# Kernel tuning notes

Measured on AMD Instinct MI355X. Metric: run time of the kernel, lower is better.

The kernel has to match this reference:

```python
import jax, jax.numpy as jnp
import numpy as np

H = 32          # phasor harmonics
DELTA0 = 7.0    # base phasor frequency
HID = 128       # hidden_dim
NEXP = 4        # num_experts
EDIM = 64       # expert_dim
NCLS = 3        # num_classes
IN_DIM = 28 * 28
ENH_DIM = HID + 2 * H  # 192


def setup_inputs() -> dict:
    key = jax.random.key(0)
    ks = jax.random.split(key, 12)
    B = 65536
    s = lambda d: 1.0 / np.sqrt(d)
    return {
        "x": jax.random.normal(ks[0], (B, 28, 28), dtype=jnp.float32),
        "W_in": jax.random.normal(ks[1], (IN_DIM, HID), dtype=jnp.float32) * s(IN_DIM),
        "b_in": jnp.zeros((HID,), dtype=jnp.float32),
        "W_gate": jax.random.normal(ks[2], (ENH_DIM, NEXP), dtype=jnp.float32) * s(ENH_DIM),
        "b_gate": jnp.zeros((NEXP,), dtype=jnp.float32),
        "W_exp": jax.random.normal(ks[3], (NEXP, ENH_DIM, EDIM), dtype=jnp.float32) * s(ENH_DIM),
        "b_exp": jnp.zeros((NEXP, EDIM), dtype=jnp.float32),
        "W_ctx": jax.random.normal(ks[4], (EDIM, HID), dtype=jnp.float32) * s(EDIM),
        "b_ctx": jnp.zeros((HID,), dtype=jnp.float32),
        "W_out": jax.random.normal(ks[5], (HID, NCLS), dtype=jnp.float32) * s(HID),
        "b_out": jnp.zeros((NCLS,), dtype=jnp.float32),
    }


def _phasor_bank(t):
    # t: [B] scalar drive per sample -> [B, 2H] cos/sin harmonic features
    freqs = DELTA0 * jnp.arange(1, H + 1, dtype=t.dtype)  # [H]
    phase = t[:, None] * freqs[None, :]                   # [B, H]
    return jnp.concatenate([jnp.cos(phase), jnp.sin(phase)], axis=-1)


def reference(x, W_in, b_in, W_gate, b_gate, W_exp, b_exp, W_ctx, b_ctx, W_out, b_out):
    B = x.shape[0]
    x_flat = x.reshape((B, -1))                                  # [B, 784]
    projected = x_flat @ W_in + b_in                             # [B, HID]
    t = jnp.mean(projected, axis=-1)                             # [B]
    temporal = _phasor_bank(t)                                   # [B, 2H]
    enhanced = jnp.concatenate([projected, temporal], axis=-1)   # [B, ENH_DIM]
    # Expert retrieval core: softmax gate over NEXP experts
    gate = jax.nn.softmax(enhanced @ W_gate + b_gate, axis=-1)   # [B, NEXP]
    expert_out = jax.nn.relu(
        jnp.einsum('bd,edh->beh', enhanced, W_exp) + b_exp[None] # [B, NEXP, EDIM]
    )
    combined = jnp.einsum('be,beh->bh', gate, expert_out)        # [B, EDIM]
    context = jnp.tanh(combined @ W_ctx + b_ctx)                 # [B, HID]
    logits = context @ W_out + b_out                             # [B, NCLS]
    return logits
```

## Files before the change

kernel.cpp:

```cpp
#include <hip/hip_runtime.h>

typedef unsigned short u16;
typedef unsigned int u32;
typedef __attribute__((ext_vector_type(8))) short short8;
typedef __attribute__((ext_vector_type(4))) float f32x4;

#define OFF_WM    0
#define OFF_WINF  3584
#define OFF_WEGF  208384
#define OFF_WCTXF 312832
#define OFF_WOUTF 329216

__device__ __forceinline__ u16 f2bf(float x) {
  union { float f; u32 u; } v; v.f = x;
  u32 r = v.u + 0x7FFFu + ((v.u >> 16) & 1u);
  return (u16)(r >> 16);
}

__global__ void prep_kernel(const float* __restrict__ W_in, const float* __restrict__ b_in,
                            const float* __restrict__ W_gate, const float* __restrict__ W_exp,
                            const float* __restrict__ W_ctx, const float* __restrict__ W_out,
                            float* __restrict__ wm, u16* __restrict__ WinF,
                            u16* __restrict__ WegF, u16* __restrict__ WctxF,
                            u16* __restrict__ WoutF) {
  int idx = blockIdx.x * 256 + threadIdx.x;
  if (idx < 801) {
    if (idx == 800) {
      float s = 0.f;
      for (int j = 0; j < 128; ++j) s += b_in[j];
      wm[800] = s * (1.f / 128.f);
    } else if (idx >= 784) {
      wm[idx] = 0.f;
    } else {
      float s = 0.f;
      for (int j = 0; j < 128; ++j) s += W_in[idx * 128 + j];
      wm[idx] = s * (1.f / 128.f);
    }
  } else if (idx < 103201) {
    int f = idx - 801;
    int j = f & 7, lane = (f >> 3) & 63, tile = f >> 9;
    int ct = tile & 7, kt = tile >> 3;
    int k = kt * 32 + ((lane >> 4) << 3) + j;
    int n = ct * 16 + (lane & 15);
    WinF[f] = (k < 784) ? f2bf(W_in[k * 128 + n]) : (u16)0;
  } else if (idx < 155425) {
    int f = idx - 103201;
    int j = f & 7, lane = (f >> 3) & 63, tile = f >> 9;
    int kt = tile / 17, ct = tile - kt * 17;
    int k = kt * 32 + ((lane >> 4) << 3) + j;
    int n = ct * 16 + (lane & 15);
    float v = 0.f;
    if (n < 256) { int e = n >> 6, h = n & 63; v = W_exp[(e * 192 + k) * 64 + h]; }
    else if (n < 260) v = W_gate[k * 4 + (n - 256)];
    WegF[f] = f2bf(v);
  } else if (idx < 163617) {
    int f = idx - 155425;
    int j = f & 7, lane = (f >> 3) & 63, tile = f >> 9;
    int ct = tile & 7, kt = tile >> 3;
    int k = kt * 32 + ((lane >> 4) << 3) + j;
    int n = ct * 16 + (lane & 15);
    WctxF[f] = f2bf(W_ctx[k * 128 + n]);
  } else if (idx < 165665) {
    int f = idx - 163617;
    int j = f & 7, lane = (f >> 3) & 63, kt = f >> 9;
    int k = kt * 32 + ((lane >> 4) << 3) + j;
    int n = lane & 15;
    WoutF[f] = (n < 3) ? f2bf(W_out[k * 3 + n]) : (u16)0;
  }
}

__global__ __launch_bounds__(256, 2)
void fused_kernel(const float* __restrict__ x,
                  const float* __restrict__ b_in, const float* __restrict__ b_gate,
                  const float* __restrict__ b_exp, const float* __restrict__ b_ctx,
                  const float* __restrict__ b_out,
                  const float* __restrict__ wm, const u16* __restrict__ WinF,
                  const u16* __restrict__ WegF, const u16* __restrict__ WctxF,
                  const u16* __restrict__ WoutF,
                  float* __restrict__ out) {
  __shared__ __align__(16) u16 smem[4 * 7680 + 8192];
  const int tid = threadIdx.x;
  const int wv = tid >> 6;
  const int ln = tid & 63;
  const int cb = ln & 15;
  const int qr = ln >> 4;
  u16* enh0 = smem + wv * 7680;
  u16* enh1 = enh0 + 3840;
  u16* cmb0 = enh0;
  u16* cmb1 = enh1;
  u16* ctx0 = enh0 + 1280;
  u16* ctx1 = enh1 + 1280;
  u16* stg  = smem + 4 * 7680;

  const int grow = blockIdx.x * 128 + wv * 32;
  const float* xr0 = x + (size_t)(grow + cb) * 784;
  const float* xr1 = xr0 + (size_t)16 * 784;

  const f32x4 vz = {0.f, 0.f, 0.f, 0.f};

  f32x4 acc0[8], acc1[8];
  #pragma unroll
  for (int i = 0; i < 8; ++i) { acc0[i] = vz; acc1[i] = vz; }
  float tp0 = 0.f, tp1 = 0.f;

  {
    const u16* src = WinF + tid * 8;
    short8 r0 = *(const short8*)(src);
    short8 r1 = *(const short8*)(src + 2048);
    *(short8*)(stg + tid * 8) = r0;
    *(short8*)(stg + 2048 + tid * 8) = r1;
  }
  __syncthreads();

  for (int kt = 0; kt < 25; ++kt) {
    const int buf = (kt & 1) << 12;
    short8 r0 = short8{0,0,0,0,0,0,0,0}, r1 = r0;
    const bool pf = (kt < 24);
    if (pf) {
      const u16* src = WinF + (size_t)(kt + 1) * 4096 + tid * 8;
      r0 = *(const short8*)(src);
      r1 = *(const short8*)(src + 2048);
    }

    const int k0 = kt * 32 + qr * 8;
    union { short8 s; u32 u[4]; } af, bf;
    {
      float4 a0 = make_float4(0.f, 0.f, 0.f, 0.f), a1 = a0;
      float4 b0 = a0, b1 = a0, m0 = a0, m1 = a0;
      if (k0 < 784) {
        a0 = *(const float4*)(xr0 + k0);
        a1 = *(const float4*)(xr0 + k0 + 4);
        b0 = *(const float4*)(xr1 + k0);
        b1 = *(const float4*)(xr1 + k0 + 4);
        m0 = *(const float4*)(wm + k0);
        m1 = *(const float4*)(wm + k0 + 4);
        tp0 += a0.x * m0.x + a0.y * m0.y + a0.z * m0.z + a0.w * m0.w
             + a1.x * m1.x + a1.y * m1.y + a1.z * m1.z + a1.w * m1.w;
        tp1 += b0.x * m0.x + b0.y * m0.y + b0.z * m0.z + b0.w * m0.w
             + b1.x * m1.x + b1.y * m1.y + b1.z * m1.z + b1.w * m1.w;
      }
      af.u[0] = (u32)f2bf(a0.x) | ((u32)f2bf(a0.y) << 16);
      af.u[1] = (u32)f2bf(a0.z) | ((u32)f2bf(a0.w) << 16);
      af.u[2] = (u32)f2bf(a1.x) | ((u32)f2bf(a1.y) << 16);
      af.u[3] = (u32)f2bf(a1.z) | ((u32)f2bf(a1.w) << 16);
      bf.u[0] = (u32)f2bf(b0.x) | ((u32)f2bf(b0.y) << 16);
      bf.u[1] = (u32)f2bf(b0.z) | ((u32)f2bf(b0.w) << 16);
      bf.u[2] = (u32)f2bf(b1.x) | ((u32)f2bf(b1.y) << 16);
      bf.u[3] = (u32)f2bf(b1.z) | ((u32)f2bf(b1.w) << 16);
    }

    short8 Bf[8];
    #pragma unroll
    for (int ct = 0; ct < 8; ++ct)
      Bf[ct] = *(const short8*)(stg + buf + ct * 512 + ln * 8);

    #pragma unroll
    for (int ct = 0; ct < 8; ++ct) {
      acc0[ct] = __builtin_amdgcn_mfma_f32_16x16x32_bf16(af.s, Bf[ct], acc0[ct], 0, 0, 0);
      acc1[ct] = __builtin_amdgcn_mfma_f32_16x16x32_bf16(bf.s, Bf[ct], acc1[ct], 0, 0, 0);
    }

    if (pf) {
      u16* dst = stg + (buf ^ 4096);
      *(short8*)(dst + tid * 8) = r0;
      *(short8*)(dst + 2048 + tid * 8) = r1;
    }
    __syncthreads();
  }

  tp0 += __shfl_xor(tp0, 16);
  tp0 += __shfl_xor(tp0, 32);
  tp1 += __shfl_xor(tp1, 16);
  tp1 += __shfl_xor(tp1, 32);
  const float mb = wm[800];
  const float t0 = tp0 + mb;
  const float t1 = tp1 + mb;

  #pragma unroll
  for (int ct = 0; ct < 8; ++ct) {
    float bi = b_in[ct * 16 + cb];
    u16* d0 = enh0 + (ct >> 1) * 640 + (ct & 1) * 16 + cb;
    u16* d1 = enh1 + (ct >> 1) * 640 + (ct & 1) * 16 + cb;
    #pragma unroll
    for (int i = 0; i < 4; ++i) {
      d0[(qr * 4 + i) * 40] = f2bf(acc0[ct][i] + bi);
      d1[(qr * 4 + i) * 40] = f2bf(acc1[ct][i] + bi);
    }
  }
  #pragma unroll
  for (int g = 0; g < 2; ++g) {
    float t = g ? t1 : t0;
    u16* eW = g ? enh1 : enh0;
    float phi = 7.f * t;
    float ss, cc, sd, cd;
    sincosf(phi * (float)(qr * 8 + 1), &ss, &cc);
    sincosf(phi, &sd, &cd);
    u16* pc = eW + 4 * 640 + cb * 40 + qr * 8;
    u16* ps = eW + 5 * 640 + cb * 40 + qr * 8;
    #pragma unroll
    for (int m = 0; m < 8; ++m) {
      pc[m] = f2bf(cc);
      ps[m] = f2bf(ss);
      float nc = cc * cd - ss * sd;
      ss = ss * cd + cc * sd;
      cc = nc;
    }
  }

  const u16* gbase = WegF + ln * 8;
  f32x4 g0 = vz, g1 = vz;
  #pragma unroll
  for (int kt = 0; kt < 6; ++kt) {
    short8 A0 = *(const short8*)(enh0 + kt * 640 + cb * 40 + qr * 8);
    short8 A1 = *(const short8*)(enh1 + kt * 640 + cb * 40 + qr * 8);
    short8 Bg = *(const short8*)(gbase + (size_t)(kt * 17 + 16) * 512);
    g0 = __builtin_amdgcn_mfma_f32_16x16x32_bf16(A0, Bg, g0, 0, 0, 0);
    g1 = __builtin_amdgcn_mfma_f32_16x16x32_bf16(A1, Bg, g1, 0, 0, 0);
  }

  float ge0[4][4], ge1[4][4];
  {
    float bg = b_gate[cb & 3];
    #pragma unroll
    for (int i = 0; i < 4; ++i) {
      {
        float gi = g0[i] + bg;
        float mx = fmaxf(gi, __shfl_xor(gi, 1));
        mx = fmaxf(mx, __shfl_xor(mx, 2));
        float ev = __expf(gi - mx);
        float sv = ev + __shfl_xor(ev, 1);
        sv += __shfl_xor(sv, 2);
        float g = ev / sv;
        int base = qr * 16;
        ge0[0][i] = __shfl(g, base + 0);
        ge0[1][i] = __shfl(g, base + 1);
        ge0[2][i] = __shfl(g, base + 2);
        ge0[3][i] = __shfl(g, base + 3);
      }
      {
        float gi = g1[i] + bg;
        float mx = fmaxf(gi, __shfl_xor(gi, 1));
        mx = fmaxf(mx, __shfl_xor(mx, 2));
        float ev = __expf(gi - mx);
        float sv = ev + __shfl_xor(ev, 1);
        sv += __shfl_xor(sv, 2);
        float g = ev / sv;
        int base = qr * 16;
        ge1[0][i] = __shfl(g, base + 0);
        ge1[1][i] = __shfl(g, base + 1);
        ge1[2][i] = __shfl(g, base + 2);
        ge1[3][i] = __shfl(g, base + 3);
      }
    }
  }

  f32x4 ae0[16], ae1[16];
  #pragma unroll
  for (int c = 0; c < 16; ++c) { ae0[c] = vz; ae1[c] = vz; }
  for (int kt = 0; kt < 6; ++kt) {
    __syncthreads();
    {
      const u16* src = WegF + (size_t)kt * 17 * 512 + tid * 8;
      short8 s0 = *(const short8*)(src);
      short8 s1 = *(const short8*)(src + 2048);
      short8 s2 = *(const short8*)(src + 4096);
      short8 s3 = *(const short8*)(src + 6144);
      *(short8*)(stg + tid * 8) = s0;
      *(short8*)(stg + 2048 + tid * 8) = s1;
      *(short8*)(stg + 4096 + tid * 8) = s2;
      *(short8*)(stg + 6144 + tid * 8) = s3;
    }
    __syncthreads();
    short8 A0 = *(const short8*)(enh0 + kt * 640 + cb * 40 + qr * 8);
    short8 A1 = *(const short8*)(enh1 + kt * 640 + cb * 40 + qr * 8);
    #pragma unroll
    for (int c = 0; c < 16; ++c) {
      short8 Bf = *(const short8*)(stg + c * 512 + ln * 8);
      ae0[c] = __builtin_amdgcn_mfma_f32_16x16x32_bf16(A0, Bf, ae0[c], 0, 0, 0);
      ae1[c] = __builtin_amdgcn_mfma_f32_16x16x32_bf16(A1, Bf, ae1[c], 0, 0, 0);
    }
  }

  f32x4 cA[4], cB[4];
  #pragma unroll
  for (int i = 0; i < 4; ++i) { cA[i] = vz; cB[i] = vz; }
  #pragma unroll
  for (int e = 0; e < 4; ++e) {
    #pragma unroll
    for (int c2 = 0; c2 < 4; ++c2) {
      float be = b_exp[e * 64 + c2 * 16 + cb];
      #pragma unroll
      for (int i = 0; i < 4; ++i) {
        cA[c2][i] += ge0[e][i] * fmaxf(ae0[e * 4 + c2][i] + be, 0.f);
        cB[c2][i] += ge1[e][i] * fmaxf(ae1[e * 4 + c2][i] + be, 0.f);
      }
    }
  }
  #pragma unroll
  for (int c2 = 0; c2 < 4; ++c2) {
    u16* d0 = cmb0 + (c2 >> 1) * 640 + (c2 & 1) * 16 + cb;
    u16* d1 = cmb1 + (c2 >> 1) * 640 + (c2 & 1) * 16 + cb;
    #pragma unroll
    for (int i = 0; i < 4; ++i) {
      d0[(qr * 4 + i) * 40] = f2bf(cA[c2][i]);
      d1[(qr * 4 + i) * 40] = f2bf(cB[c2][i]);
    }
  }

  __syncthreads();
  {
    const u16* src = WctxF + tid * 8;
    short8 s0 = *(const short8*)(src);
    short8 s1 = *(const short8*)(src + 2048);
    short8 s2 = *(const short8*)(src + 4096);
    short8 s3 = *(const short8*)(src + 6144);
    *(short8*)(stg + tid * 8) = s0;
    *(short8*)(stg + 2048 + tid * 8) = s1;
    *(short8*)(stg + 4096 + tid * 8) = s2;
    *(short8*)(stg + 6144 + tid * 8) = s3;
  }
  __syncthreads();
  f32x4 c30[8], c31[8];
  #pragma unroll
  for (int i = 0; i < 8; ++i) { c30[i] = vz; c31[i] = vz; }
  #pragma unroll
  for (int kt = 0; kt < 2; ++kt) {
    short8 A0 = *(const short8*)(cmb0 + kt * 640 + cb * 40 + qr * 8);
    short8 A1 = *(const short8*)(cmb1 + kt * 640 + cb * 40 + qr * 8);
    #pragma unroll
    for (int ct = 0; ct < 8; ++ct) {
      short8 Bf = *(const short8*)(stg + (kt * 8 + ct) * 512 + ln * 8);
      c30[ct] = __builtin_amdgcn_mfma_f32_16x16x32_bf16(A0, Bf, c30[ct], 0, 0, 0);
      c31[ct] = __builtin_amdgcn_mfma_f32_16x16x32_bf16(A1, Bf, c31[ct], 0, 0, 0);
    }
  }
  #pragma unroll
  for (int ct = 0; ct < 8; ++ct) {
    float bc = b_ctx[ct * 16 + cb];
    u16* d0 = ctx0 + ct * 16 + cb;
    u16* d1 = ctx1 + ct * 16 + cb;
    #pragma unroll
    for (int i = 0; i < 4; ++i) {
      float v0 = c30[ct][i] + bc;
      float e0 = __expf(2.f * v0);
      d0[(qr * 4 + i) * 136] = f2bf(1.f - 2.f / (e0 + 1.f));
      float v1 = c31[ct][i] + bc;
      float e1 = __expf(2.f * v1);
      d1[(qr * 4 + i) * 136] = f2bf(1.f - 2.f / (e1 + 1.f));
    }
  }

  __syncthreads();
  {
    short8 s0 = *(const short8*)(WoutF + tid * 8);
    *(short8*)(stg + tid * 8) = s0;
  }
  __syncthreads();
  f32x4 a40 = vz, a41 = vz;
  #pragma unroll
  for (int kt = 0; kt < 4; ++kt) {
    short8 A0 = *(const short8*)(ctx0 + cb * 136 + kt * 32 + qr * 8);
    short8 A1 = *(const short8*)(ctx1 + cb * 136 + kt * 32 + qr * 8);
    short8 Bf = *(const short8*)(stg + kt * 512 + ln * 8);
    a40 = __builtin_amdgcn_mfma_f32_16x16x32_bf16(A0, Bf, a40, 0, 0, 0);
    a41 = __builtin_amdgcn_mfma_f32_16x16x32_bf16(A1, Bf, a41, 0, 0, 0);
  }
  if (cb < 3) {
    float bo = b_out[cb];
    #pragma unroll
    for (int i = 0; i < 4; ++i) {
      out[(size_t)(grow + qr * 4 + i) * 3 + cb] = a40[i] + bo;
      out[(size_t)(grow + 16 + qr * 4 + i) * 3 + cb] = a41[i] + bo;
    }
  }
}

extern "C" void kernel_launch(void* const* d_in, const int* in_sizes, int n_in,
                              void* d_out, int out_size, void* d_ws, size_t ws_size,
                              hipStream_t stream) {
  const float* x      = (const float*)d_in[0];
  const float* W_in   = (const float*)d_in[1];
  const float* b_in   = (const float*)d_in[2];
  const float* W_gate = (const float*)d_in[3];
  const float* b_gate = (const float*)d_in[4];
  const float* W_exp  = (const float*)d_in[5];
  const float* b_exp  = (const float*)d_in[6];
  const float* W_ctx  = (const float*)d_in[7];
  const float* b_ctx  = (const float*)d_in[8];
  const float* W_out  = (const float*)d_in[9];
  const float* b_out  = (const float*)d_in[10];
  float* out = (float*)d_out;

  char* ws = (char*)d_ws;
  float* wm  = (float*)(ws + OFF_WM);
  u16* WinF  = (u16*)(ws + OFF_WINF);
  u16* WegF  = (u16*)(ws + OFF_WEGF);
  u16* WctxF = (u16*)(ws + OFF_WCTXF);
  u16* WoutF = (u16*)(ws + OFF_WOUTF);

  const int B = in_sizes[0] / 784;
  prep_kernel<<<648, 256, 0, stream>>>(W_in, b_in, W_gate, W_exp, W_ctx, W_out,
                                       wm, WinF, WegF, WctxF, WoutF);
  fused_kernel<<<B / 128, 256, 0, stream>>>(x, b_in, b_gate, b_exp, b_ctx, b_out,
                                            wm, WinF, WegF, WctxF, WoutF, out);
}
```

Baseline: 328.1 us.

## Pre-convert x to bf16 MFMA layout in a separate high-occupancy kernel

Adds a prepx kernel that reads fp32 x once and writes it as bf16 into workspace, laid out in MFMA A-fragment order. The same kernel computes the per-row mean projection t. The fused kernel then loads ready-made bf16 fragments instead of converting fp32 and accumulating t inside its low-occupancy main loop. The cost is an extra write and read of the roughly 100MB bf16 copy plus one more launch. The old fused path is kept as a fallback when the workspace is too small.

```diff
diff --git a/kernel.cpp b/kernel.cpp
--- a/kernel.cpp
+++ b/kernel.cpp
@@ -10,6 +10,8 @@
 #define OFF_WEGF  208384
 #define OFF_WCTXF 312832
 #define OFF_WOUTF 329216
+#define OFF_T     524288
+#define OFF_XF    1048576
 
 __device__ __forceinline__ u16 f2bf(float x) {
   union { float f; u32 u; } v; v.f = x;
@@ -69,15 +71,52 @@
   }
 }
 
+__global__ __launch_bounds__(256, 8)
+void prepx_kernel(const float* __restrict__ x, const float* __restrict__ wm,
+                  u16* __restrict__ xf, float* __restrict__ t, int nrt) {
+  const int rt = blockIdx.x * 4 + (threadIdx.x >> 6);
+  if (rt >= nrt) return;
+  const int ln = threadIdx.x & 63;
+  const int cb = ln & 15;
+  const int qr = ln >> 4;
+  const int row = rt * 16 + cb;
+  const float* xr = x + (size_t)row * 784;
+  u16* dst = xf + ((size_t)rt * 25 * 64 + ln) * 8;
+
+  float part = 0.f;
+  for (int kt = 0; kt < 25; ++kt) {
+    const int k0 = kt * 32 + qr * 8;
+    union { short8 s; u32 u[4]; } af;
+    if (k0 < 784) {
+      float4 a0 = *(const float4*)(xr + k0);
+      float4 a1 = *(const float4*)(xr + k0 + 4);
+      const float4 m0 = *(const float4*)(wm + k0);
+      const float4 m1 = *(const float4*)(wm + k0 + 4);
+      part += a0.x * m0.x + a0.y * m0.y + a0.z * m0.z + a0.w * m0.w
+            + a1.x * m1.x + a1.y * m1.y + a1.z * m1.z + a1.w * m1.w;
+      af.u[0] = (u32)f2bf(a0.x) | ((u32)f2bf(a0.y) << 16);
+      af.u[1] = (u32)f2bf(a0.z) | ((u32)f2bf(a0.w) << 16);
+      af.u[2] = (u32)f2bf(a1.x) | ((u32)f2bf(a1.y) << 16);
+      af.u[3] = (u32)f2bf(a1.z) | ((u32)f2bf(a1.w) << 16);
+    } else {
+      af.u[0] = 0; af.u[1] = 0; af.u[2] = 0; af.u[3] = 0;
+    }
+    *(short8*)(dst + kt * 512) = af.s;
+  }
+  part += __shfl_xor(part, 16);
+  part += __shfl_xor(part, 32);
+  if (ln < 16) t[row] = part;
+}
+
 __global__ __launch_bounds__(256, 2)
-void fused_kernel(const float* __restrict__ x,
-                  const float* __restrict__ b_in, const float* __restrict__ b_gate,
-                  const float* __restrict__ b_exp, const float* __restrict__ b_ctx,
-                  const float* __restrict__ b_out,
-                  const float* __restrict__ wm, const u16* __restrict__ WinF,
-                  const u16* __restrict__ WegF, const u16* __restrict__ WctxF,
-                  const u16* __restrict__ WoutF,
-                  float* __restrict__ out) {
+void fused_kernel_xf(const u16* __restrict__ xf, const float* __restrict__ t,
+                     const float* __restrict__ b_in, const float* __restrict__ b_gate,
+                     const float* __restrict__ b_exp, const float* __restrict__ b_ctx,
+                     const float* __restrict__ b_out,
+                     const float* __restrict__ wm, const u16* __restrict__ WinF,
+                     const u16* __restrict__ WegF, const u16* __restrict__ WctxF,
+                     const u16* __restrict__ WoutF,
+                     float* __restrict__ out) {
   __shared__ __align__(16) u16 smem[4 * 7680 + 8192];
   const int tid = threadIdx.x;
   const int wv = tid >> 6;
@@ -93,15 +132,15 @@
   u16* stg  = smem + 4 * 7680;
 
   const int grow = blockIdx.x * 128 + wv * 32;
-  const float* xr0 = x + (size_t)(grow + cb) * 784;
-  const float* xr1 = xr0 + (size_t)16 * 784;
+  const int rtA = grow >> 4;
+  const u16* xfA = xf + ((size_t)rtA * 25 * 64 + ln) * 8;
+  const u16* xfB = xfA + (size_t)25 * 512;
 
   const f32x4 vz = {0.f, 0.f, 0.f, 0.f};
 
   f32x4 acc0[8], acc1[8];
   #pragma unroll
   for (int i = 0; i < 8; ++i) { acc0[i] = vz; acc1[i] = vz; }
-  float tp0 = 0.f, tp1 = 0.f;
 
   {
     const u16* src = WinF + tid * 8;
@@ -122,32 +161,8 @@
       r1 = *(const short8*)(src + 2048);
     }
 
-    const int k0 = kt * 32 + qr * 8;
-    union { short8 s; u32 u[4]; } af, bf;
-    {
-      float4 a0 = make_float4(0.f, 0.f, 0.f, 0.f), a1 = a0;
-      float4 b0 = a0, b1 = a0, m0 = a0, m1 = a0;
-      if (k0 < 784) {
-        a0 = *(const float4*)(xr0 + k0);
-        a1 = *(const float4*)(xr0 + k0 + 4);
-        b0 = *(const float4*)(xr1 + k0);
-        b1 = *(const float4*)(xr1 + k0 + 4);
-        m0 = *(const float4*)(wm + k0);
-        m1 = *(const float4*)(wm + k0 + 4);
-        tp0 += a0.x * m0.x + a0.y * m0.y + a0.z * m0.z + a0.w * m0.w
-             + a1.x * m1.x + a1.y * m1.y + a1.z * m1.z + a1.w * m1.w;
-        tp1 += b0.x * m0.x + b0.y * m0.y + b0.z * m0.z + b0.w * m0.w
-             + b1.x * m1.x + b1.y * m1.y + b1.z * m1.z + b1.w * m1.w;
-      }
-      af.u[0] = (u32)f2bf(a0.x) | ((u32)f2bf(a0.y) << 16);
-      af.u[1] = (u32)f2bf(a0.z) | ((u32)f2bf(a0.w) << 16);
-      af.u[2] = (u32)f2bf(a1.x) | ((u32)f2bf(a1.y) << 16);
-      af.u[3] = (u32)f2bf(a1.z) | ((u32)f2bf(a1.w) << 16);
-      bf.u[0] = (u32)f2bf(b0.x) | ((u32)f2bf(b0.y) << 16);
-      bf.u[1] = (u32)f2bf(b0.z) | ((u32)f2bf(b0.w) << 16);
-      bf.u[2] = (u32)f2bf(b1.x) | ((u32)f2bf(b1.y) << 16);
-      bf.u[3] = (u32)f2bf(b1.z) | ((u32)f2bf(b1.w) << 16);
-    }
+    short8 A0 = *(const short8*)(xfA + kt * 512);
+    short8 A1 = *(const short8*)(xfB + kt * 512);
 
     short8 Bf[8];
     #pragma unroll
@@ -156,8 +171,8 @@
 
     #pragma unroll
     for (int ct = 0; ct < 8; ++ct) {
-      acc0[ct] = __builtin_amdgcn_mfma_f32_16x16x32_bf16(af.s, Bf[ct], acc0[ct], 0, 0, 0);
-      acc1[ct] = __builtin_amdgcn_mfma_f32_16x16x32_bf16(bf.s, Bf[ct], acc1[ct], 0, 0, 0);
+      acc0[ct] = __builtin_amdgcn_mfma_f32_16x16x32_bf16(A0, Bf[ct], acc0[ct], 0, 0, 0);
+      acc1[ct] = __builtin_amdgcn_mfma_f32_16x16x32_bf16(A1, Bf[ct], acc1[ct], 0, 0, 0);
     }
 
     if (pf) {
@@ -168,13 +183,9 @@
     __syncthreads();
   }
 
-  tp0 += __shfl_xor(tp0, 16);
-  tp0 += __shfl_xor(tp0, 32);
-  tp1 += __shfl_xor(tp1, 16);
-  tp1 += __shfl_xor(tp1, 32);
   const float mb = wm[800];
-  const float t0 = tp0 + mb;
-  const float t1 = tp1 + mb;
+  const float t0 = t[grow + cb] + mb;
+  const float t1 = t[grow + 16 + cb] + mb;
 
   #pragma unroll
   for (int ct = 0; ct < 8; ++ct) {
@@ -189,9 +200,9 @@
   }
   #pragma unroll
   for (int g = 0; g < 2; ++g) {
-    float t = g ? t1 : t0;
+    float t_ = g ? t1 : t0;
     u16* eW = g ? enh1 : enh0;
-    float phi = 7.f * t;
+    float phi = 7.f * t_;
     float ss, cc, sd, cd;
     sincosf(phi * (float)(qr * 8 + 1), &ss, &cc);
     sincosf(phi, &sd, &cd);
@@ -375,6 +386,312 @@
   }
 }
 
+__global__ __launch_bounds__(256, 2)
+void fused_kernel_x(const float* __restrict__ x,
+                    const float* __restrict__ b_in, const float* __restrict__ b_gate,
+                    const float* __restrict__ b_exp, const float* __restrict__ b_ctx,
+                    const float* __restrict__ b_out,
+                    const float* __restrict__ wm, const u16* __restrict__ WinF,
+                    const u16* __restrict__ WegF, const u16* __restrict__ WctxF,
+                    const u16* __restrict__ WoutF,
+                    float* __restrict__ out) {
+  __shared__ __align__(16) u16 smem[4 * 7680 + 8192];
+  const int tid = threadIdx.x;
+  const int wv = tid >> 6;
+  const int ln = tid & 63;
+  const int cb = ln & 15;
+  const int qr = ln >> 4;
+  u16* enh0 = smem + wv * 7680;
+  u16* enh1 = enh0 + 3840;
+  u16* cmb0 = enh0;
+  u16* cmb1 = enh1;
+  u16* ctx0 = enh0 + 1280;
+  u16* ctx1 = enh1 + 1280;
+  u16* stg  = smem + 4 * 7680;
+
+  const int grow = blockIdx.x * 128 + wv * 32;
+  const float* xr0 = x + (size_t)(grow + cb) * 784;
+  const float* xr1 = xr0 + (size_t)16 * 784;
+
+  const f32x4 vz = {0.f, 0.f, 0.f, 0.f};
+
+  f32x4 acc0[8], acc1[8];
+  #pragma unroll
+  for (int i = 0; i < 8; ++i) { acc0[i] = vz; acc1[i] = vz; }
+  float tp0 = 0.f, tp1 = 0.f;
+
+  {
+    const u16* src = WinF + tid * 8;
+    short8 r0 = *(const short8*)(src);
+    short8 r1 = *(const short8*)(src + 2048);
+    *(short8*)(stg + tid * 8) = r0;
+    *(short8*)(stg + 2048 + tid * 8) = r1;
+  }
+  __syncthreads();
+
+  for (int kt = 0; kt < 25; ++kt) {
+    const int buf = (kt & 1) << 12;
+    short8 r0 = short8{0,0,0,0,0,0,0,0}, r1 = r0;
+    const bool pf = (kt < 24);
+    if (pf) {
+      const u16* src = WinF + (size_t)(kt + 1) * 4096 + tid * 8;
+      r0 = *(const short8*)(src);
+      r1 = *(const short8*)(src + 2048);
+    }
+
+    const int k0 = kt * 32 + qr * 8;
+    union { short8 s; u32 u[4]; } af, bf;
+    {
+      float4 a0 = make_float4(0.f, 0.f, 0.f, 0.f), a1 = a0;
+      float4 b0 = a0, b1 = a0, m0 = a0, m1 = a0;
+      if (k0 < 784) {
+        a0 = *(const float4*)(xr0 + k0);
+        a1 = *(const float4*)(xr0 + k0 + 4);
+        b0 = *(const float4*)(xr1 + k0);
+        b1 = *(const float4*)(xr1 + k0 + 4);
+        m0 = *(const float4*)(wm + k0);
+        m1 = *(const float4*)(wm + k0 + 4);
+        tp0 += a0.x * m0.x + a0.y * m0.y + a0.z * m0.z + a0.w * m0.w
+             + a1.x * m1.x + a1.y * m1.y + a1.z * m1.z + a1.w * m1.w;
+        tp1 += b0.x * m0.x + b0.y * m0.y + b0.z * m0.z + b0.w * m0.w
+             + b1.x * m1.x + b1.y * m1.y + b1.z * m1.z + b1.w * m1.w;
+      }
+      af.u[0] = (u32)f2bf(a0.x) | ((u32)f2bf(a0.y) << 16);
+      af.u[1] = (u32)f2bf(a0.z) | ((u32)f2bf(a0.w) << 16);
+      af.u[2] = (u32)f2bf(a1.x) | ((u32)f2bf(a1.y) << 16);
+      af.u[3] = (u32)f2bf(a1.z) | ((u32)f2bf(a1.w) << 16);
+      bf.u[0] = (u32)f2bf(b0.x) | ((u32)f2bf(b0.y) << 16);
+      bf.u[1] = (u32)f2bf(b0.z) | ((u32)f2bf(b0.w) << 16);
+      bf.u[2] = (u32)f2bf(b1.x) | ((u32)f2bf(b1.y) << 16);
+      bf.u[3] = (u32)f2bf(b1.z) | ((u32)f2bf(b1.w) << 16);
+    }
+
+    short8 Bf[8];
+    #pragma unroll
+    for (int ct = 0; ct < 8; ++ct)
+      Bf[ct] = *(const short8*)(stg + buf + ct * 512 + ln * 8);
+
+    #pragma unroll
+    for (int ct = 0; ct < 8; ++ct) {
+      acc0[ct] = __builtin_amdgcn_mfma_f32_16x16x32_bf16(af.s, Bf[ct], acc0[ct], 0, 0, 0);
+      acc1[ct] = __builtin_amdgcn_mfma_f32_16x16x32_bf16(bf.s, Bf[ct], acc1[ct], 0, 0, 0);
+    }
+
+    if (pf) {
+      u16* dst = stg + (buf ^ 4096);
+      *(short8*)(dst + tid * 8) = r0;
+      *(short8*)(dst + 2048 + tid * 8) = r1;
+    }
+    __syncthreads();
+  }
+
+  tp0 += __shfl_xor(tp0, 16);
+  tp0 += __shfl_xor(tp0, 32);
+  tp1 += __shfl_xor(tp1, 16);
+  tp1 += __shfl_xor(tp1, 32);
+  const float mb = wm[800];
+  const float t0 = tp0 + mb;
+  const float t1 = tp1 + mb;
+
+  #pragma unroll
+  for (int ct = 0; ct < 8; ++ct) {
+    float bi = b_in[ct * 16 + cb];
+    u16* d0 = enh0 + (ct >> 1) * 640 + (ct & 1) * 16 + cb;
+    u16* d1 = enh1 + (ct >> 1) * 640 + (ct & 1) * 16 + cb;
+    #pragma unroll
+    for (int i = 0; i < 4; ++i) {
+      d0[(qr * 4 + i) * 40] = f2bf(acc0[ct][i] + bi);
+      d1[(qr * 4 + i) * 40] = f2bf(acc1[ct][i] + bi);
+    }
+  }
+  #pragma unroll
+  for (int g = 0; g < 2; ++g) {
+    float t_ = g ? t1 : t0;
+    u16* eW = g ? enh1 : enh0;
+    float phi = 7.f * t_;
+    float ss, cc, sd, cd;
+    sincosf(phi * (float)(qr * 8 + 1), &ss, &cc);
+    sincosf(phi, &sd, &cd);
+    u16* pc = eW + 4 * 640 + cb * 40 + qr * 8;
+    u16* ps = eW + 5 * 640 + cb * 40 + qr * 8;
+    #pragma unroll
+    for (int m = 0; m < 8; ++m) {
+      pc[m] = f2bf(cc);
+      ps[m] = f2bf(ss);
+      float nc = cc * cd - ss * sd;
+      ss = ss * cd + cc * sd;
+      cc = nc;
+    }
+  }
+
+  const u16* gbase = WegF + ln * 8;
+  f32x4 g0 = vz, g1 = vz;
+  #pragma unroll
+  for (int kt = 0; kt < 6; ++kt) {
+    short8 A0 = *(const short8*)(enh0 + kt * 640 + cb * 40 + qr * 8);
+    short8 A1 = *(const short8*)(enh1 + kt * 640 + cb * 40 + qr * 8);
+    short8 Bg = *(const short8*)(gbase + (size_t)(kt * 17 + 16) * 512);
+    g0 = __builtin_amdgcn_mfma_f32_16x16x32_bf16(A0, Bg, g0, 0, 0, 0);
+    g1 = __builtin_amdgcn_mfma_f32_16x16x32_bf16(A1, Bg, g1, 0, 0, 0);
+  }
+
+  float ge0[4][4], ge1[4][4];
+  {
+    float bg = b_gate[cb & 3];
+    #pragma unroll
+    for (int i = 0; i < 4; ++i) {
+      {
+        float gi = g0[i] + bg;
+        float mx = fmaxf(gi, __shfl_xor(gi, 1));
+        mx = fmaxf(mx, __shfl_xor(mx, 2));
+        float ev = __expf(gi - mx);
+        float sv = ev + __shfl_xor(ev, 1);
+        sv += __shfl_xor(sv, 2);
+        float g = ev / sv;
+        int base = qr * 16;
+        ge0[0][i] = __shfl(g, base + 0);
+        ge0[1][i] = __shfl(g, base + 1);
+        ge0[2][i] = __shfl(g, base + 2);
+        ge0[3][i] = __shfl(g, base + 3);
+      }
+      {
+        float gi = g1[i] + bg;
+        float mx = fmaxf(gi, __shfl_xor(gi, 1));
+        mx = fmaxf(mx, __shfl_xor(mx, 2));
+        float ev = __expf(gi - mx);
+        float sv = ev + __shfl_xor(ev, 1);
+        sv += __shfl_xor(sv, 2);
+        float g = ev / sv;
+        int base = qr * 16;
+        ge1[0][i] = __shfl(g, base + 0);
+        ge1[1][i] = __shfl(g, base + 1);
+        ge1[2][i] = __shfl(g, base + 2);
+        ge1[3][i] = __shfl(g, base + 3);
+      }
+    }
+  }
+
+  f32x4 ae0[16], ae1[16];
+  #pragma unroll
+  for (int c = 0; c < 16; ++c) { ae0[c] = vz; ae1[c] = vz; }
+  for (int kt = 0; kt < 6; ++kt) {
+    __syncthreads();
+    {
+      const u16* src = WegF + (size_t)kt * 17 * 512 + tid * 8;
+      short8 s0 = *(const short8*)(src);
+      short8 s1 = *(const short8*)(src + 2048);
+      short8 s2 = *(const short8*)(src + 4096);
+      short8 s3 = *(const short8*)(src + 6144);
+      *(short8*)(stg + tid * 8) = s0;
+      *(short8*)(stg + 2048 + tid * 8) = s1;
+      *(short8*)(stg + 4096 + tid * 8) = s2;
+      *(short8*)(stg + 6144 + tid * 8) = s3;
+    }
+    __syncthreads();
+    short8 A0 = *(const short8*)(enh0 + kt * 640 + cb * 40 + qr * 8);
+    short8 A1 = *(const short8*)(enh1 + kt * 640 + cb * 40 + qr * 8);
+    #pragma unroll
+    for (int c = 0; c < 16; ++c) {
+      short8 Bf = *(const short8*)(stg + c * 512 + ln * 8);
+      ae0[c] = __builtin_amdgcn_mfma_f32_16x16x32_bf16(A0, Bf, ae0[c], 0, 0, 0);
+      ae1[c] = __builtin_amdgcn_mfma_f32_16x16x32_bf16(A1, Bf, ae1[c], 0, 0, 0);
+    }
+  }
+
+  f32x4 cA[4], cB[4];
+  #pragma unroll
+  for (int i = 0; i < 4; ++i) { cA[i] = vz; cB[i] = vz; }
+  #pragma unroll
+  for (int e = 0; e < 4; ++e) {
+    #pragma unroll
+    for (int c2 = 0; c2 < 4; ++c2) {
+      float be = b_exp[e * 64 + c2 * 16 + cb];
+      #pragma unroll
+      for (int i = 0; i < 4; ++i) {
+        cA[c2][i] += ge0[e][i] * fmaxf(ae0[e * 4 + c2][i] + be, 0.f);
+        cB[c2][i] += ge1[e][i] * fmaxf(ae1[e * 4 + c2][i] + be, 0.f);
+      }
+    }
+  }
+  #pragma unroll
+  for (int c2 = 0; c2 < 4; ++c2) {
+    u16* d0 = cmb0 + (c2 >> 1) * 640 + (c2 & 1) * 16 + cb;
+    u16* d1 = cmb1 + (c2 >> 1) * 640 + (c2 & 1) * 16 + cb;
+    #pragma unroll
+    for (int i = 0; i < 4; ++i) {
+      d0[(qr * 4 + i) * 40] = f2bf(cA[c2][i]);
+      d1[(qr * 4 + i) * 40] = f2bf(cB[c2][i]);
+    }
+  }
+
+  __syncthreads();
+  {
+    const u16* src = WctxF + tid * 8;
+    short8 s0 = *(const short8*)(src);
+    short8 s1 = *(const short8*)(src + 2048);
+    short8 s2 = *(const short8*)(src + 4096);
+    short8 s3 = *(const short8*)(src + 6144);
+    *(short8*)(stg + tid * 8) = s0;
+    *(short8*)(stg + 2048 + tid * 8) = s1;
+    *(short8*)(stg + 4096 + tid * 8) = s2;
+    *(short8*)(stg + 6144 + tid * 8) = s3;
+  }
+  __syncthreads();
+  f32x4 c30[8], c31[8];
+  #pragma unroll
+  for (int i = 0; i < 8; ++i) { c30[i] = vz; c31[i] = vz; }
+  #pragma unroll
+  for (int kt = 0; kt < 2; ++kt) {
+    short8 A0 = *(const short8*)(cmb0 + kt * 640 + cb * 40 + qr * 8);
+    short8 A1 = *(const short8*)(cmb1 + kt * 640 + cb * 40 + qr * 8);
+    #pragma unroll
+    for (int ct = 0; ct < 8; ++ct) {
+      short8 Bf = *(const short8*)(stg + (kt * 8 + ct) * 512 + ln * 8);
+      c30[ct] = __builtin_amdgcn_mfma_f32_16x16x32_bf16(A0, Bf, c30[ct], 0, 0, 0);
+      c31[ct] = __builtin_amdgcn_mfma_f32_16x16x32_bf16(A1, Bf, c31[ct], 0, 0, 0);
+    }
+  }
+  #pragma unroll
+  for (int ct = 0; ct < 8; ++ct) {
+    float bc = b_ctx[ct * 16 + cb];
+    u16* d0 = ctx0 + ct * 16 + cb;
+    u16* d1 = ctx1 + ct * 16 + cb;
+    #pragma unroll
+    for (int i = 0; i < 4; ++i) {
+      float v0 = c30[ct][i] + bc;
+      float e0 = __expf(2.f * v0);
+      d0[(qr * 4 + i) * 136] = f2bf(1.f - 2.f / (e0 + 1.f));
+      float v1 = c31[ct][i] + bc;
+      float e1 = __expf(2.f * v1);
+      d1[(qr * 4 + i) * 136] = f2bf(1.f - 2.f / (e1 + 1.f));
+    }
+  }
+
+  __syncthreads();
+  {
+    short8 s0 = *(const short8*)(WoutF + tid * 8);
+    *(short8*)(stg + tid * 8) = s0;
+  }
+  __syncthreads();
+  f32x4 a40 = vz, a41 = vz;
+  #pragma unroll
+  for (int kt = 0; kt < 4; ++kt) {
+    short8 A0 = *(const short8*)(ctx0 + cb * 136 + kt * 32 + qr * 8);
+    short8 A1 = *(const short8*)(ctx1 + cb * 136 + kt * 32 + qr * 8);
+    short8 Bf = *(const short8*)(stg + kt * 512 + ln * 8);
+    a40 = __builtin_amdgcn_mfma_f32_16x16x32_bf16(A0, Bf, a40, 0, 0, 0);
+    a41 = __builtin_amdgcn_mfma_f32_16x16x32_bf16(A1, Bf, a41, 0, 0, 0);
+  }
+  if (cb < 3) {
+    float bo = b_out[cb];
+    #pragma unroll
+    for (int i = 0; i < 4; ++i) {
+      out[(size_t)(grow + qr * 4 + i) * 3 + cb] = a40[i] + bo;
+      out[(size_t)(grow + 16 + qr * 4 + i) * 3 + cb] = a41[i] + bo;
+    }
+  }
+}
+
 extern "C" void kernel_launch(void* const* d_in, const int* in_sizes, int n_in,
                               void* d_out, int out_size, void* d_ws, size_t ws_size,
                               hipStream_t stream) {
@@ -397,10 +714,22 @@
   u16* WegF  = (u16*)(ws + OFF_WEGF);
   u16* WctxF = (u16*)(ws + OFF_WCTXF);
   u16* WoutF = (u16*)(ws + OFF_WOUTF);
+  float* t   = (float*)(ws + OFF_T);
+  u16* xf    = (u16*)(ws + OFF_XF);
 
   const int B = in_sizes[0] / 784;
+  const int nrt = B / 16;
+  const size_t need = (size_t)OFF_XF + (size_t)nrt * 25 * 64 * 8 * sizeof(u16);
+
   prep_kernel<<<648, 256, 0, stream>>>(W_in, b_in, W_gate, W_exp, W_ctx, W_out,
                                        wm, WinF, WegF, WctxF, WoutF);
-  fused_kernel<<<B / 128, 256, 0, stream>>>(x, b_in, b_gate, b_exp, b_ctx, b_out,
-                                            wm, WinF, WegF, WctxF, WoutF, out);
+  if (ws_size >= need) {
+    prepx_kernel<<<(nrt + 3) / 4, 256, 0, stream>>>(x, wm, xf, t, nrt);
+    fused_kernel_xf<<<B / 128, 256, 0, stream>>>(xf, t, b_in, b_gate, b_exp, b_ctx,
+                                                 b_out, wm, WinF, WegF, WctxF, WoutF,
+                                                 out);
+  } else {
+    fused_kernel_x<<<B / 128, 256, 0, stream>>>(x, b_in, b_gate, b_exp, b_ctx, b_out,
+                                                wm, WinF, WegF, WctxF, WoutF, out);
+  }
 }
```

After: 383.7 us. +17.0%, slower.
